# Kernel tuning notes

Measured on AMD Instinct MI355X. Metric: run time of the kernel, lower is better.

## Reference

```python
import jax, jax.numpy as jnp
import numpy as np

N_CLASS = 20          # foreground classes (VOC)
SCORE_THR = 0.05
NMS_THR = 0.3
IMG_H, IMG_W = 600, 800
R = 2000              # number of proposed ROIs


def setup_inputs() -> dict:
    key = jax.random.key(0)
    k1, k2, k3, k4, k5 = jax.random.split(key, 5)
    # well-formed proposal boxes (y1, x1, y2, x2)
    cy = jax.random.uniform(k1, (R,), minval=0.0, maxval=float(IMG_H))
    cx = jax.random.uniform(k2, (R,), minval=0.0, maxval=float(IMG_W))
    hw = jax.random.uniform(k3, (R, 2), minval=20.0, maxval=200.0)
    h, w = hw[:, 0], hw[:, 1]
    boxes = jnp.stack([
        jnp.clip(cy - 0.5 * h, 0.0, IMG_H),
        jnp.clip(cx - 0.5 * w, 0.0, IMG_W),
        jnp.clip(cy + 0.5 * h, 0.0, IMG_H),
        jnp.clip(cx + 0.5 * w, 0.0, IMG_W),
    ], axis=1).astype(jnp.float32)
    loc = (0.2 * jax.random.normal(k4, (R, 4 * (N_CLASS + 1)))).astype(jnp.float32)
    score = (2.0 * jax.random.normal(k5, (R, N_CLASS + 1))).astype(jnp.float32)
    return {
        "proposed_roi_bboxes": boxes,
        "predicted_roi_loc": loc,
        "predicted_roi_score": score,
        "img_height": IMG_H,
        "img_width": IMG_W,
    }


def _pairwise_iou(b):
    # b: [N, 4] in (y1, x1, y2, x2); IoU is invariant to axis order
    tl = jnp.maximum(b[:, None, :2], b[None, :, :2])
    br = jnp.minimum(b[:, None, 2:], b[None, :, 2:])
    wh = jnp.clip(br - tl, 0.0)
    inter = wh[..., 0] * wh[..., 1]
    area = (b[:, 2] - b[:, 0]) * (b[:, 3] - b[:, 1])
    union = area[:, None] + area[None, :] - inter
    return inter / jnp.maximum(union, 1e-9)


def _nms_keep(boxes_sorted, valid_sorted, thr):
    # boxes sorted by descending score; returns keep mask [N]
    N = boxes_sorted.shape[0]
    iou = _pairwise_iou(boxes_sorted)          # [N, N]
    idx = jnp.arange(N)
    def body(suppressed, i):
        keep_i = valid_sorted[i] & (~suppressed[i])
        suppressed = suppressed | (keep_i & (iou[i] > thr) & (idx > i))
        return suppressed, keep_i
    _, keep = jax.lax.scan(body, jnp.zeros((N,), bool), idx)
    return keep


def _detect(proposed_roi_bboxes, predicted_roi_loc, predicted_roi_score, H, W):
    Rn = proposed_roi_bboxes.shape[0]
    C1 = N_CLASS + 1
    b = proposed_roi_bboxes
    loc = predicted_roi_loc.reshape(Rn, C1, 4)
    # Utility.loc2bbox (y1,x1,y2,x2 <-> cy,cx,h,w)
    src_h = b[:, 2] - b[:, 0]
    src_w = b[:, 3] - b[:, 1]
    src_cy = b[:, 0] + 0.5 * src_h
    src_cx = b[:, 1] + 0.5 * src_w
    dy, dx, dh, dw = loc[..., 0], loc[..., 1], loc[..., 2], loc[..., 3]
    cy = dy * src_h[:, None] + src_cy[:, None]
    cx = dx * src_w[:, None] + src_cx[:, None]
    hh = jnp.exp(dh) * src_h[:, None]
    ww = jnp.exp(dw) * src_w[:, None]
    boxes = jnp.stack([cy - 0.5 * hh, cx - 0.5 * ww,
                       cy + 0.5 * hh, cx + 0.5 * ww], axis=-1)  # [R, C1, 4]
    # clamp: even coords (y) to [0,H], odd coords (x) to [0,W]
    boxes = jnp.stack([
        jnp.clip(boxes[..., 0], 0.0, H),
        jnp.clip(boxes[..., 1], 0.0, W),
        jnp.clip(boxes[..., 2], 0.0, H),
        jnp.clip(boxes[..., 3], 0.0, W),
    ], axis=-1)
    prob = jax.nn.softmax(predicted_roi_score, axis=1)          # [R, C1]

    # foreground classes 1..N_CLASS -> leading class axis [C, R, ...]
    fg_boxes = jnp.transpose(boxes[:, 1:, :], (1, 0, 2))        # [C, R, 4]
    fg_prob = prob[:, 1:].T                                     # [C, R]
    valid = fg_prob > SCORE_THR
    sort_key = jnp.where(valid, fg_prob, -jnp.inf)
    order = jnp.argsort(-sort_key, axis=1)                      # [C, R]
    boxes_s = jnp.take_along_axis(fg_boxes, order[..., None], axis=1)
    prob_s = jnp.take_along_axis(fg_prob, order, axis=1)
    valid_s = jnp.take_along_axis(valid, order, axis=1)

    keep = jax.vmap(_nms_keep, in_axes=(0, 0, None))(boxes_s, valid_s, NMS_THR)  # [C, R] bool

    km = keep.astype(boxes_s.dtype)
    out = jnp.concatenate([boxes_s, prob_s[..., None]], axis=-1) * km[..., None]  # [C, R, 5]
    labels = jnp.arange(1, N_CLASS + 1, dtype=boxes_s.dtype)[:, None] * km        # [C, R]
    return out, labels, keep


def reference(proposed_roi_bboxes, predicted_roi_loc, predicted_roi_score,
              img_height, img_width):
    out, labels, keep = _detect(proposed_roi_bboxes, predicted_roi_loc,
                                predicted_roi_score, float(img_height), float(img_width))
    return out, labels, keep
```

## Files before the change

kernel.cpp:

```cpp
#include <hip/hip_runtime.h>
#include <cstdint>

#pragma clang fp contract(off)

#define R_N   2000
#define C1    21
#define NCLS  20
#define MAXFV 512
#define OUT_LBL   200000
#define OUT_KEEP  240000
#define FMARGIN   4.0f

__device__ __forceinline__ double read_dim(const void* p) {
  int iv = *(const int*)p;
  if (iv >= 1 && iv <= 1000000) return (double)iv;
  float fv = *(const float*)p;
  if (fv >= 1.0f && fv <= 1000000.0f) return (double)fv;
  return *(const double*)p;
}

__global__ __launch_bounds__(256) void prep2_kernel(
    const float* __restrict__ score, const float* __restrict__ loc,
    double* __restrict__ tab4, double* __restrict__ prob_t)
{
  int tid = blockIdx.x * 256 + threadIdx.x;
  if (tid < 40000) {
    int r = tid % R_N, c = tid / R_N;
    const float* l4 = loc + r * 84 + (c + 1) * 4;
    double* o = tab4 + (size_t)(c * R_N + r) * 4;
    o[0] = (double)l4[0];
    o[1] = (double)l4[1];
    o[2] = exp((double)l4[2]);
    o[3] = exp((double)l4[3]);
  } else if (tid >= 40960 && tid < 40960 + R_N) {
    int r = tid - 40960;
    const float* sc = score + r * C1;
    double m = (double)sc[0];
    #pragma unroll
    for (int k = 1; k < C1; ++k) m = fmax(m, (double)sc[k]);
    double e[C1]; double s = 0.0;
    #pragma unroll
    for (int k = 0; k < C1; ++k) { e[k] = exp((double)sc[k] - m); s += e[k]; }
    #pragma unroll
    for (int c = 0; c < NCLS; ++c) prob_t[c * R_N + r] = e[c + 1] / s;
  }
}

__global__ __launch_bounds__(256) void decode_sort2_kernel(
    const float* __restrict__ rois, const float* __restrict__ loc,
    const float* __restrict__ score,
    const void* __restrict__ hptr, const void* __restrict__ wptr,
    float* __restrict__ out,
    const double* __restrict__ tab4, const double* __restrict__ prob_t,
    float4* __restrict__ fbox4, double4* __restrict__ dbox4,
    float* __restrict__ farea, float* __restrict__ sprobg,
    int* __restrict__ vcls, int mode)
{
  __shared__ double sbd[R_N][4];
  __shared__ ulonglong2 keys[2048];
  __shared__ double klist64[2][64][5];
  __shared__ float  klist32[2][64][5];
  __shared__ int kcnt[2];
  __shared__ int wsum[4];

  const int cls = blockIdx.x;
  const int t = threadIdx.x;
  const int lane = t & 63, wid = t >> 6;
  const double H = read_dim(hptr), W = read_dim(wptr);

  ulonglong2 rk[8];
  int vmask = 0;
  #pragma unroll
  for (int u = 0; u < 8; ++u) {
    int r = t + 256 * u;
    rk[u] = make_ulonglong2(0ull, 0ull);
    if (r < R_N) {
      double p, dy, dx, eh, ew;
      if (mode) {
        p = prob_t[cls * R_N + r];
        const double* o = tab4 + (size_t)(cls * R_N + r) * 4;
        dy = o[0]; dx = o[1]; eh = o[2]; ew = o[3];
      } else {
        const float* sc = score + r * C1;
        double m = (double)sc[0];
        #pragma unroll
        for (int k = 1; k < C1; ++k) m = fmax(m, (double)sc[k]);
        double s = 0.0;
        #pragma unroll
        for (int k = 0; k < C1; ++k) s += exp((double)sc[k] - m);
        const float* l4 = loc + r * 84 + (cls + 1) * 4;
        p = exp((double)sc[cls + 1] - m) / s;
        dy = (double)l4[0]; dx = (double)l4[1];
        eh = exp((double)l4[2]); ew = exp((double)l4[3]);
      }
      double b0 = (double)rois[r*4+0], b1 = (double)rois[r*4+1];
      double b2 = (double)rois[r*4+2], b3 = (double)rois[r*4+3];
      double sh  = b2 - b0,       sw  = b3 - b1;
      double scy = b0 + 0.5*sh,   scx = b1 + 0.5*sw;
      double cy = dy*sh + scy,    cx = dx*sw + scx;
      double hh = eh*sh,          ww = ew*sw;
      double y1 = fmin(fmax(cy - 0.5*hh, 0.0), H);
      double x1 = fmin(fmax(cx - 0.5*ww, 0.0), W);
      double y2 = fmin(fmax(cy + 0.5*hh, 0.0), H);
      double x2 = fmin(fmax(cx + 0.5*ww, 0.0), W);
      sbd[r][0]=y1; sbd[r][1]=x1; sbd[r][2]=y2; sbd[r][3]=x2;
      if (p > 0.05) {
        rk[u] = make_ulonglong2((unsigned long long)__double_as_longlong(p),
                                (unsigned long long)(unsigned int)(~r));
        vmask |= 1 << u;
      }
    }
  }

  int cnt = __popc(vmask);
  int x = cnt;
  #pragma unroll
  for (int off = 1; off < 64; off <<= 1) {
    int y = __shfl_up(x, off);
    if (lane >= off) x += y;
  }
  if (lane == 63) wsum[wid] = x;
  __syncthreads();
  int woff = 0;
  #pragma unroll
  for (int w2 = 0; w2 < 4; ++w2) { int s = wsum[w2]; if (w2 < wid) woff += s; }
  const int V = wsum[0] + wsum[1] + wsum[2] + wsum[3];
  int pos = woff + x - cnt;
  #pragma unroll
  for (int u = 0; u < 8; ++u)
    if ((vmask >> u) & 1) keys[pos++] = rk[u];

  int NSORT = 64; while (NSORT < V) NSORT <<= 1;
  for (int j = V + t; j < NSORT; j += 256)
    keys[j] = make_ulonglong2(0ull, (unsigned long long)(unsigned int)(~(unsigned)j));
  __syncthreads();

  for (int k = 2; k <= NSORT; k <<= 1) {
    for (int js = k >> 1; js > 0; js >>= 1) {
      for (int p = t; p < (NSORT >> 1); p += 256) {
        int i = ((p & ~(js - 1)) << 1) | (p & (js - 1));
        int j = i | js;
        ulonglong2 a = keys[i], b = keys[j];
        bool altb = (a.x < b.x) || (a.x == b.x && a.y < b.y);
        if (altb == ((i & k) == 0)) { keys[i] = b; keys[j] = a; }
      }
      __syncthreads();
    }
  }

  if (mode && V <= MAXFV) {
    for (int j = t; j < V; j += 256) {
      int idx = (int)(~(unsigned)keys[j].y);
      double a0=sbd[idx][0], a1=sbd[idx][1], a2=sbd[idx][2], a3=sbd[idx][3];
      int g = cls * MAXFV + j;
      fbox4[g] = make_float4((float)a0, (float)a1, (float)a2, (float)a3);
      dbox4[g] = make_double4(a0, a1, a2, a3);
      farea[g] = (float)((a2-a0)*(a3-a1));
      sprobg[g] = (float)__longlong_as_double((long long)keys[j].x);
    }
    if (t == 0) vcls[cls] = V;
    return;
  }
  if (mode && t == 0) vcls[cls] = V;

  int   idx8[8];
  float fx0[8], fx1[8], fx2[8], fx3[8], far5[8], pr[8];
  unsigned am = 0, km = 0;
  #pragma unroll
  for (int q = 0; q < 8; ++q) {
    int j = t + 256 * q;
    fx0[q]=fx1[q]=fx2[q]=fx3[q]=far5[q]=pr[q]=0.f; idx8[q]=0;
    if (j < V) {
      int idx = (int)(~(unsigned)keys[j].y);
      idx8[q] = idx;
      double a0=sbd[idx][0], a1=sbd[idx][1], a2=sbd[idx][2], a3=sbd[idx][3];
      fx0[q]=(float)a0; fx1[q]=(float)a1; fx2[q]=(float)a2; fx3[q]=(float)a3;
      far5[q]=(float)((a2-a0)*(a3-a1));
      pr[q]=(float)__longlong_as_double((long long)keys[j].x);
      am |= 1u << q;
    }
  }

  #pragma unroll
  for (int q = 0; q < 8; ++q) {
    if (256 * q >= V) break;
    for (int sub = 0; sub < 4; ++sub) {
      const int ch = 4 * q + sub;
      if (64 * ch >= V) break;
      const int buf = ch & 1;
      if (wid == sub) {
        const int s = 64 * ch + lane;
        bool a = ((am >> q) & 1u) != 0u;
        int myidx = idx8[q];
        float f0=fx0[q], f1=fx1[q], f2=fx2[q], f3=fx3[q], fa=far5[q];
        unsigned long long m = __ballot(a);
        unsigned long long kept = 0;
        while (m) {
          int i = __ffsll(m) - 1;
          m &= m - 1;
          kept |= 1ull << i;
          float k0=__shfl(f0,i), k1=__shfl(f1,i), k2=__shfl(f2,i), k3=__shfl(f3,i), ka=__shfl(fa,i);
          bool aliveL = ((m >> lane) & 1ull) != 0ull;
          float ty=fmaxf(k0,f0), tx=fmaxf(k1,f1);
          float by=fminf(k2,f2), bz=fminf(k3,f3);
          float w0=fmaxf(by-ty,0.f), w1=fmaxf(bz-tx,0.f);
          float inter=w0*w1;
          float uni=fmaxf(ka+fa-inter, 1e-9f);
          float rhs=0.3f*uni;
          bool kill = aliveL && (inter > rhs + FMARGIN);
          bool amb  = aliveL && !kill && (inter > rhs - FMARGIN);
          if (__any(amb)) {
            int kidx = __shfl(myidx, i);
            double b0=sbd[kidx][0], b1=sbd[kidx][1], b2=sbd[kidx][2], b3=sbd[kidx][3];
            double bar=(b2-b0)*(b3-b1);
            if (amb) {
              double a0=sbd[myidx][0], a1=sbd[myidx][1], a2=sbd[myidx][2], a3=sbd[myidx][3];
              double aar=(a2-a0)*(a3-a1);
              double ty_=fmax(b0,a0), tx_=fmax(b1,a1);
              double by_=fmin(b2,a2), bz_=fmin(b3,a3);
              double w0_=fmax(by_-ty_,0.0), w1_=fmax(bz_-tx_,0.0);
              double in_=w0_*w1_;
              double un_=bar+aar-in_;
              if (in_/fmax(un_,1e-9) > 0.3) kill = true;
            }
          }
          m &= ~__ballot(kill);
        }
        am &= ~(1u << q);
        if ((kept >> lane) & 1ull) {
          km |= 1u << q;
          int kpos = (int)__popcll(kept & ((1ull << lane) - 1ull));
          double a0=sbd[myidx][0], a1=sbd[myidx][1], a2=sbd[myidx][2], a3=sbd[myidx][3];
          klist64[buf][kpos][0]=a0; klist64[buf][kpos][1]=a1;
          klist64[buf][kpos][2]=a2; klist64[buf][kpos][3]=a3;
          klist64[buf][kpos][4]=(a2-a0)*(a3-a1);
          klist32[buf][kpos][0]=f0; klist32[buf][kpos][1]=f1;
          klist32[buf][kpos][2]=f2; klist32[buf][kpos][3]=f3; klist32[buf][kpos][4]=fa;
        }
        if (lane == 0) kcnt[buf] = (int)__popcll(kept);
      }
      __syncthreads();
      const int nk = kcnt[buf];
      const int jmin = 64 * (ch + 1);
      for (int n = 0; n < nk; ++n) {
        float k0=klist32[buf][n][0], k1=klist32[buf][n][1];
        float k2=klist32[buf][n][2], k3=klist32[buf][n][3], ka=klist32[buf][n][4];
        #pragma unroll
        for (int q2 = 0; q2 < 8; ++q2) {
          if (256 * q2 >= V) break;
          int j2 = t + 256 * q2;
          if (((am >> q2) & 1u) && j2 >= jmin) {
            float ty=fmaxf(k0,fx0[q2]), tx=fmaxf(k1,fx1[q2]);
            float by=fminf(k2,fx2[q2]), bz=fminf(k3,fx3[q2]);
            float w0=fmaxf(by-ty,0.f), w1=fmaxf(bz-tx,0.f);
            float inter=w0*w1;
            float uni=fmaxf(ka+far5[q2]-inter, 1e-9f);
            float rhs=0.3f*uni;
            if (inter > rhs + FMARGIN) {
              am &= ~(1u << q2);
            } else if (inter > rhs - FMARGIN) {
              int idx = idx8[q2];
              double a0=sbd[idx][0], a1=sbd[idx][1], a2=sbd[idx][2], a3=sbd[idx][3];
              double ar_=(a2-a0)*(a3-a1);
              double b0=klist64[buf][n][0], b1=klist64[buf][n][1];
              double b2=klist64[buf][n][2], b3=klist64[buf][n][3], br=klist64[buf][n][4];
              double ty_=fmax(b0,a0), tx_=fmax(b1,a1);
              double by_=fmin(b2,a2), bz_=fmin(b3,a3);
              double w0_=fmax(by_-ty_,0.0), w1_=fmax(bz_-tx_,0.0);
              double in_=w0_*w1_;
              double un_=br+ar_-in_;
              if (in_/fmax(un_,1e-9) > 0.3) am &= ~(1u << q2);
            }
          }
        }
      }
    }
  }

  #pragma unroll
  for (int u = 0; u < 8; ++u) {
    int j = t + 256 * u;
    if (j < R_N) {
      int row = cls * R_N + j;
      bool k = ((km >> u) & 1u) != 0u;
      out[row*5+0] = k ? fx0[u] : 0.f;
      out[row*5+1] = k ? fx1[u] : 0.f;
      out[row*5+2] = k ? fx2[u] : 0.f;
      out[row*5+3] = k ? fx3[u] : 0.f;
      out[row*5+4] = k ? pr[u]  : 0.f;
      out[OUT_LBL  + row] = k ? (float)(cls + 1) : 0.f;
      out[OUT_KEEP + row] = k ? 1.f : 0.f;
    }
  }
}

__global__ __launch_bounds__(256) void build_kernel(
    const float4* __restrict__ fbox4, const float* __restrict__ farea,
    const double4* __restrict__ dbox4, const int* __restrict__ vcls,
    unsigned long long* __restrict__ kw)
{
  const int cls = blockIdx.x;
  const int V = vcls[cls];
  if (V > MAXFV) return;
  int n = blockIdx.y * 256 + threadIdx.x;
  int c = 0;
  #pragma unroll
  for (int cc = 1; cc < 8; ++cc) if (n >= 32*cc*(cc+1)) c = cc;
  int rem = n - 32*c*(c+1);
  int jq = rem / (c + 1);
  int j = 64*c + jq;
  int w = rem - jq*(c+1);
  if (j >= V) return;

  const float4* fb = fbox4 + cls * MAXFV;
  const float*  fa = farea + cls * MAXFV;
  float4 mb = fb[j];
  float  ma = fa[j];
  int i0 = 64*w;
  int i1 = min(i0 + 64, j);
  unsigned long long acc = 0ull;
  #pragma unroll 8
  for (int i = i0; i < i1; ++i) {
    float4 bb = fb[i]; float ba = fa[i];
    float ty=fmaxf(bb.x,mb.x), tx=fmaxf(bb.y,mb.y);
    float by=fminf(bb.z,mb.z), bz=fminf(bb.w,mb.w);
    float w0=fmaxf(by-ty,0.f), w1=fmaxf(bz-tx,0.f);
    float inter=w0*w1;
    float uni=fmaxf(ba+ma-inter, 1e-9f);
    float rhs=0.3f*uni;
    bool kill = inter > rhs + FMARGIN;
    if (!kill && inter > rhs - FMARGIN) {
      double4 bd = dbox4[cls*MAXFV + i];
      double4 md = dbox4[cls*MAXFV + j];
      double bar=(bd.z-bd.x)*(bd.w-bd.y);
      double dar=(md.z-md.x)*(md.w-md.y);
      double ty_=fmax(bd.x,md.x), tx_=fmax(bd.y,md.y);
      double by_=fmin(bd.z,md.z), bz_=fmin(bd.w,md.w);
      double w0_=fmax(by_-ty_,0.0), w1_=fmax(bz_-tx_,0.0);
      double in_=w0_*w1_;
      double un_=bar+dar-in_;
      kill = in_/fmax(un_,1e-9) > 0.3;
    }
    acc |= (unsigned long long)(kill ? 1 : 0) << (i & 63);
  }
  kw[(size_t)(cls*MAXFV + j)*8 + w] = acc;
}

__global__ __launch_bounds__(256) void scan_kernel(
    float* __restrict__ out,
    const float4* __restrict__ fbox4, const float* __restrict__ sprobg,
    const unsigned long long* __restrict__ kw, const int* __restrict__ vcls)
{
  __shared__ unsigned long long ckill[2][8][256];
  __shared__ unsigned long long keptm[8];
  const int cls = blockIdx.x;
  const int V = vcls[cls];
  if (V > MAXFV) return;
  const int t = threadIdx.x, lane = t & 63, wid = t >> 6;

  unsigned long long ckq[2] = {0ull, 0ull};
  unsigned am = 0;
  #pragma unroll
  for (int q = 0; q < 2; ++q) {
    int j = t + 256*q;
    if (j < V) {
      am |= 1u << q;
      const unsigned long long* src = kw + (size_t)(cls*MAXFV + j)*8;
      int c = wid + 4*q;
      for (int w = 0; w < c; ++w) ckill[q][w][t] = src[w];
      ckq[q] = src[c];
    }
  }

  unsigned km = 0;
  #pragma unroll
  for (int q = 0; q < 2; ++q) {
    if (256*q >= V) break;
    for (int sub = 0; sub < 4; ++sub) {
      const int ch = 4*q + sub;
      if (64*ch >= V) break;
      if (wid == sub) {
        bool a = ((am >> q) & 1u) != 0u;
        unsigned long long m = __ballot(a);
        unsigned long long kept = 0ull;
        while (m) {
          int i = __ffsll(m) - 1;
          unsigned long long bit = 1ull << i;
          kept |= bit; m &= ~bit;
          bool kill = ((ckq[q] >> i) & 1ull) != 0ull;
          m &= ~__ballot(kill);
        }
        am &= ~(1u << q);
        if ((kept >> lane) & 1ull) km |= 1u << q;
        if (lane == 0) keptm[ch] = kept;
      }
      __syncthreads();
      unsigned long long K = keptm[ch];
      #pragma unroll
      for (int q2 = 0; q2 < 2; ++q2) {
        if (256*q2 >= V) break;
        if (((am >> q2) & 1u) && (wid + 4*q2) > ch) {
          if (ckill[q2][ch][t] & K) am &= ~(1u << q2);
        }
      }
    }
  }

  #pragma unroll
  for (int u = 0; u < 8; ++u) {
    int j = t + 256*u;
    if (j < R_N) {
      int row = cls*R_N + j;
      bool k = (u < 2) && ((km >> u) & 1u);
      float v0=0.f, v1=0.f, v2=0.f, v3=0.f, v4=0.f;
      if (k) {
        float4 b = fbox4[cls*MAXFV + j];
        v0=b.x; v1=b.y; v2=b.z; v3=b.w; v4=sprobg[cls*MAXFV + j];
      }
      out[row*5+0]=v0; out[row*5+1]=v1; out[row*5+2]=v2; out[row*5+3]=v3; out[row*5+4]=v4;
      out[OUT_LBL  + row] = k ? (float)(cls + 1) : 0.f;
      out[OUT_KEEP + row] = k ? 1.f : 0.f;
    }
  }
}

extern "C" void kernel_launch(void* const* d_in, const int* in_sizes, int n_in,
                              void* d_out, int out_size, void* d_ws, size_t ws_size,
                              hipStream_t stream) {
  const float* rois  = (const float*)d_in[0];
  const float* loc   = (const float*)d_in[1];
  const float* score = (const float*)d_in[2];
  const void*  hp    = d_in[3];
  const void*  wp    = d_in[4];
  float* out = (float*)d_out;

  char* wsb = (char*)d_ws;
  double*  tab4   = (double*)(wsb + 0);
  double*  prob_t = (double*)(wsb + 1280000);
  float4*  fbox4  = (float4*)(wsb + 1600000);
  double4* dbox4  = (double4*)(wsb + 1763840);
  float*   farea  = (float*)(wsb + 2091520);
  float*   sprob  = (float*)(wsb + 2132480);
  unsigned long long* kw = (unsigned long long*)(wsb + 2173440);
  int*     vcls   = (int*)(wsb + 2828800);
  const size_t WS_NEED = 2828880;

  if (ws_size >= WS_NEED) {
    prep2_kernel<<<dim3(168), dim3(256), 0, stream>>>(score, loc, tab4, prob_t);
    decode_sort2_kernel<<<dim3(NCLS), dim3(256), 0, stream>>>(
        rois, loc, score, hp, wp, out, tab4, prob_t,
        fbox4, dbox4, farea, sprob, vcls, 1);
    build_kernel<<<dim3(NCLS, 9), dim3(256), 0, stream>>>(fbox4, farea, dbox4, vcls, kw);
    scan_kernel<<<dim3(NCLS), dim3(256), 0, stream>>>(out, fbox4, sprob, kw, vcls);
  } else {
    decode_sort2_kernel<<<dim3(NCLS), dim3(256), 0, stream>>>(
        rois, loc, score, hp, wp, out, (const double*)nullptr, (const double*)nullptr,
        (float4*)nullptr, (double4*)nullptr, (float*)nullptr, (float*)nullptr,
        (int*)nullptr, 0);
  }
}
```

Baseline: 57.56 us.

## Move box decode into prep kernel and replace bitonic sort with rank counting

Box decoding and clipping for every (class, ROI) pair moves into the wide prep kernel, which now writes full double4 boxes to a workspace table. The per-class kernel skips the shared-memory bitonic sort on the fast path (V <= 512). Instead, each valid key computes its rank by comparing against all other valid keys and scatters its box and probability straight to the sorted slot. This removes the many barrier-separated sort stages and the serial decode from the 20-block kernel, at the cost of O(V^2) shared-memory comparisons per class and an extra global read of the decoded boxes.

```diff
diff --git a/kernel.cpp b/kernel.cpp
--- a/kernel.cpp
+++ b/kernel.cpp
@@ -19,19 +19,30 @@
   return *(const double*)p;
 }
 
-__global__ __launch_bounds__(256) void prep2_kernel(
-    const float* __restrict__ score, const float* __restrict__ loc,
-    double* __restrict__ tab4, double* __restrict__ prob_t)
+__global__ __launch_bounds__(256) void prep3_kernel(
+    const float* __restrict__ rois, const float* __restrict__ loc,
+    const float* __restrict__ score,
+    const void* __restrict__ hptr, const void* __restrict__ wptr,
+    double4* __restrict__ dbox_all, double* __restrict__ prob_t)
 {
   int tid = blockIdx.x * 256 + threadIdx.x;
   if (tid < 40000) {
     int r = tid % R_N, c = tid / R_N;
+    const double H = read_dim(hptr), W = read_dim(wptr);
     const float* l4 = loc + r * 84 + (c + 1) * 4;
-    double* o = tab4 + (size_t)(c * R_N + r) * 4;
-    o[0] = (double)l4[0];
-    o[1] = (double)l4[1];
-    o[2] = exp((double)l4[2]);
-    o[3] = exp((double)l4[3]);
+    double dy = (double)l4[0], dx = (double)l4[1];
+    double eh = exp((double)l4[2]), ew = exp((double)l4[3]);
+    double b0 = (double)rois[r*4+0], b1 = (double)rois[r*4+1];
+    double b2 = (double)rois[r*4+2], b3 = (double)rois[r*4+3];
+    double sh  = b2 - b0,       sw  = b3 - b1;
+    double scy = b0 + 0.5*sh,   scx = b1 + 0.5*sw;
+    double cy = dy*sh + scy,    cx = dx*sw + scx;
+    double hh = eh*sh,          ww = ew*sw;
+    double y1 = fmin(fmax(cy - 0.5*hh, 0.0), H);
+    double x1 = fmin(fmax(cx - 0.5*ww, 0.0), W);
+    double y2 = fmin(fmax(cy + 0.5*hh, 0.0), H);
+    double x2 = fmin(fmax(cx + 0.5*ww, 0.0), W);
+    dbox_all[c * R_N + r] = make_double4(y1, x1, y2, x2);
   } else if (tid >= 40960 && tid < 40960 + R_N) {
     int r = tid - 40960;
     const float* sc = score + r * C1;
@@ -46,13 +57,13 @@
   }
 }
 
-__global__ __launch_bounds__(256) void decode_sort2_kernel(
+__global__ __launch_bounds__(256) void compact_rank_kernel(
     const float* __restrict__ rois, const float* __restrict__ loc,
     const float* __restrict__ score,
     const void* __restrict__ hptr, const void* __restrict__ wptr,
     float* __restrict__ out,
-    const double* __restrict__ tab4, const double* __restrict__ prob_t,
-    float4* __restrict__ fbox4, double4* __restrict__ dbox4,
+    const double4* __restrict__ dbox_all, const double* __restrict__ prob_t,
+    float4* __restrict__ fbox4, double4* __restrict__ dbox4s,
     float* __restrict__ farea, float* __restrict__ sprobg,
     int* __restrict__ vcls, int mode)
 {
@@ -66,7 +77,6 @@
   const int cls = blockIdx.x;
   const int t = threadIdx.x;
   const int lane = t & 63, wid = t >> 6;
-  const double H = read_dim(hptr), W = read_dim(wptr);
 
   ulonglong2 rk[8];
   int vmask = 0;
@@ -75,11 +85,9 @@
     int r = t + 256 * u;
     rk[u] = make_ulonglong2(0ull, 0ull);
     if (r < R_N) {
-      double p, dy, dx, eh, ew;
+      double p;
       if (mode) {
         p = prob_t[cls * R_N + r];
-        const double* o = tab4 + (size_t)(cls * R_N + r) * 4;
-        dy = o[0]; dx = o[1]; eh = o[2]; ew = o[3];
       } else {
         const float* sc = score + r * C1;
         double m = (double)sc[0];
@@ -88,22 +96,8 @@
         double s = 0.0;
         #pragma unroll
         for (int k = 0; k < C1; ++k) s += exp((double)sc[k] - m);
-        const float* l4 = loc + r * 84 + (cls + 1) * 4;
         p = exp((double)sc[cls + 1] - m) / s;
-        dy = (double)l4[0]; dx = (double)l4[1];
-        eh = exp((double)l4[2]); ew = exp((double)l4[3]);
-      }
-      double b0 = (double)rois[r*4+0], b1 = (double)rois[r*4+1];
-      double b2 = (double)rois[r*4+2], b3 = (double)rois[r*4+3];
-      double sh  = b2 - b0,       sw  = b3 - b1;
-      double scy = b0 + 0.5*sh,   scx = b1 + 0.5*sw;
-      double cy = dy*sh + scy,    cx = dx*sw + scx;
-      double hh = eh*sh,          ww = ew*sw;
-      double y1 = fmin(fmax(cy - 0.5*hh, 0.0), H);
-      double x1 = fmin(fmax(cx - 0.5*ww, 0.0), W);
-      double y2 = fmin(fmax(cy + 0.5*hh, 0.0), H);
-      double x2 = fmin(fmax(cx + 0.5*ww, 0.0), W);
-      sbd[r][0]=y1; sbd[r][1]=x1; sbd[r][2]=y2; sbd[r][3]=x2;
+      }
       if (p > 0.05) {
         rk[u] = make_ulonglong2((unsigned long long)__double_as_longlong(p),
                                 (unsigned long long)(unsigned int)(~r));
@@ -130,6 +124,65 @@
   for (int u = 0; u < 8; ++u)
     if ((vmask >> u) & 1) keys[pos++] = rk[u];
 
+  if (mode && V <= MAXFV) {
+    __syncthreads();
+    #pragma unroll
+    for (int q = 0; q < 2; ++q) {
+      int j = t + 256 * q;
+      if (j < V) {
+        ulonglong2 kj = keys[j];
+        int rank = 0;
+        int i = 0;
+        for (; i + 4 <= V; i += 4) {
+          ulonglong2 g0 = keys[i], g1 = keys[i+1], g2 = keys[i+2], g3 = keys[i+3];
+          rank += ((g0.x > kj.x) || (g0.x == kj.x && g0.y > kj.y)) ? 1 : 0;
+          rank += ((g1.x > kj.x) || (g1.x == kj.x && g1.y > kj.y)) ? 1 : 0;
+          rank += ((g2.x > kj.x) || (g2.x == kj.x && g2.y > kj.y)) ? 1 : 0;
+          rank += ((g3.x > kj.x) || (g3.x == kj.x && g3.y > kj.y)) ? 1 : 0;
+        }
+        for (; i < V; ++i) {
+          ulonglong2 gi = keys[i];
+          rank += ((gi.x > kj.x) || (gi.x == kj.x && gi.y > kj.y)) ? 1 : 0;
+        }
+        int idx = (int)(~(unsigned)kj.y);
+        double4 bd = dbox_all[cls * R_N + idx];
+        int g = cls * MAXFV + rank;
+        fbox4[g]  = make_float4((float)bd.x, (float)bd.y, (float)bd.z, (float)bd.w);
+        dbox4s[g] = bd;
+        farea[g]  = (float)((bd.z - bd.x) * (bd.w - bd.y));
+        sprobg[g] = (float)__longlong_as_double((long long)kj.x);
+      }
+    }
+    if (t == 0) vcls[cls] = V;
+    return;
+  }
+  if (mode && t == 0) vcls[cls] = V;
+
+  #pragma unroll
+  for (int u = 0; u < 8; ++u) {
+    int r = t + 256 * u;
+    if (r < R_N) {
+      if (mode) {
+        double4 bd = dbox_all[cls * R_N + r];
+        sbd[r][0]=bd.x; sbd[r][1]=bd.y; sbd[r][2]=bd.z; sbd[r][3]=bd.w;
+      } else {
+        const double H = read_dim(hptr), W = read_dim(wptr);
+        const float* l4 = loc + r * 84 + (cls + 1) * 4;
+        double dy = (double)l4[0], dx = (double)l4[1];
+        double eh = exp((double)l4[2]), ew = exp((double)l4[3]);
+        double b0 = (double)rois[r*4+0], b1 = (double)rois[r*4+1];
+        double b2 = (double)rois[r*4+2], b3 = (double)rois[r*4+3];
+        double sh  = b2 - b0,       sw  = b3 - b1;
+        double scy = b0 + 0.5*sh,   scx = b1 + 0.5*sw;
+        double cy = dy*sh + scy,    cx = dx*sw + scx;
+        double hh = eh*sh,          ww = ew*sw;
+        sbd[r][0] = fmin(fmax(cy - 0.5*hh, 0.0), H);
+        sbd[r][1] = fmin(fmax(cx - 0.5*ww, 0.0), W);
+        sbd[r][2] = fmin(fmax(cy + 0.5*hh, 0.0), H);
+        sbd[r][3] = fmin(fmax(cx + 0.5*ww, 0.0), W);
+      }
+    }
+  }
   int NSORT = 64; while (NSORT < V) NSORT <<= 1;
   for (int j = V + t; j < NSORT; j += 256)
     keys[j] = make_ulonglong2(0ull, (unsigned long long)(unsigned int)(~(unsigned)j));
@@ -147,21 +200,6 @@
       __syncthreads();
     }
   }
-
-  if (mode && V <= MAXFV) {
-    for (int j = t; j < V; j += 256) {
-      int idx = (int)(~(unsigned)keys[j].y);
-      double a0=sbd[idx][0], a1=sbd[idx][1], a2=sbd[idx][2], a3=sbd[idx][3];
-      int g = cls * MAXFV + j;
-      fbox4[g] = make_float4((float)a0, (float)a1, (float)a2, (float)a3);
-      dbox4[g] = make_double4(a0, a1, a2, a3);
-      farea[g] = (float)((a2-a0)*(a3-a1));
-      sprobg[g] = (float)__longlong_as_double((long long)keys[j].x);
-    }
-    if (t == 0) vcls[cls] = V;
-    return;
-  }
-  if (mode && t == 0) vcls[cls] = V;
 
   int   idx8[8];
   float fx0[8], fx1[8], fx2[8], fx3[8], far5[8], pr[8];
@@ -296,7 +334,7 @@
 
 __global__ __launch_bounds__(256) void build_kernel(
     const float4* __restrict__ fbox4, const float* __restrict__ farea,
-    const double4* __restrict__ dbox4, const int* __restrict__ vcls,
+    const double4* __restrict__ dbox4s, const int* __restrict__ vcls,
     unsigned long long* __restrict__ kw)
 {
   const int cls = blockIdx.x;
@@ -330,8 +368,8 @@
     float rhs=0.3f*uni;
     bool kill = inter > rhs + FMARGIN;
     if (!kill && inter > rhs - FMARGIN) {
-      double4 bd = dbox4[cls*MAXFV + i];
-      double4 md = dbox4[cls*MAXFV + j];
+      double4 bd = dbox4s[cls*MAXFV + i];
+      double4 md = dbox4s[cls*MAXFV + j];
       double bar=(bd.z-bd.x)*(bd.w-bd.y);
       double dar=(md.z-md.x)*(md.w-md.y);
       double ty_=fmax(bd.x,md.x), tx_=fmax(bd.y,md.y);
@@ -435,26 +473,27 @@
   float* out = (float*)d_out;
 
   char* wsb = (char*)d_ws;
-  double*  tab4   = (double*)(wsb + 0);
-  double*  prob_t = (double*)(wsb + 1280000);
-  float4*  fbox4  = (float4*)(wsb + 1600000);
-  double4* dbox4  = (double4*)(wsb + 1763840);
-  float*   farea  = (float*)(wsb + 2091520);
-  float*   sprob  = (float*)(wsb + 2132480);
+  double4* dbox_all = (double4*)(wsb + 0);
+  double*  prob_t   = (double*)(wsb + 1280000);
+  float4*  fbox4    = (float4*)(wsb + 1600000);
+  double4* dbox4s   = (double4*)(wsb + 1763840);
+  float*   farea    = (float*)(wsb + 2091520);
+  float*   sprob    = (float*)(wsb + 2132480);
   unsigned long long* kw = (unsigned long long*)(wsb + 2173440);
-  int*     vcls   = (int*)(wsb + 2828800);
+  int*     vcls     = (int*)(wsb + 2828800);
   const size_t WS_NEED = 2828880;
 
   if (ws_size >= WS_NEED) {
-    prep2_kernel<<<dim3(168), dim3(256), 0, stream>>>(score, loc, tab4, prob_t);
-    decode_sort2_kernel<<<dim3(NCLS), dim3(256), 0, stream>>>(
-        rois, loc, score, hp, wp, out, tab4, prob_t,
-        fbox4, dbox4, farea, sprob, vcls, 1);
-    build_kernel<<<dim3(NCLS, 9), dim3(256), 0, stream>>>(fbox4, farea, dbox4, vcls, kw);
+    prep3_kernel<<<dim3(168), dim3(256), 0, stream>>>(rois, loc, score, hp, wp,
+                                                      dbox_all, prob_t);
+    compact_rank_kernel<<<dim3(NCLS), dim3(256), 0, stream>>>(
+        rois, loc, score, hp, wp, out, dbox_all, prob_t,
+        fbox4, dbox4s, farea, sprob, vcls, 1);
+    build_kernel<<<dim3(NCLS, 9), dim3(256), 0, stream>>>(fbox4, farea, dbox4s, vcls, kw);
     scan_kernel<<<dim3(NCLS), dim3(256), 0, stream>>>(out, fbox4, sprob, kw, vcls);
   } else {
-    decode_sort2_kernel<<<dim3(NCLS), dim3(256), 0, stream>>>(
-        rois, loc, score, hp, wp, out, (const double*)nullptr, (const double*)nullptr,
+    compact_rank_kernel<<<dim3(NCLS), dim3(256), 0, stream>>>(
+        rois, loc, score, hp, wp, out, (const double4*)nullptr, (const double*)nullptr,
         (float4*)nullptr, (double4*)nullptr, (float*)nullptr, (float*)nullptr,
         (int*)nullptr, 0);
   }
```

Result: slower. 86.19 us (+49.8%).
